# Performance work log

Hardware: AMD Instinct MI355X
Metric: run time of the kernel (lower is better)

The kernel has to match this reference:

```python
import jax, jax.numpy as jnp
import numpy as np

NUM_HEADS = 8
FREQ_RATIO = 0.5


def _resize_bilinear(img, out_h, out_w):
    """Bilinear resize of last two dims, matching torch interpolate align_corners=False."""
    in_h, in_w = img.shape[-2], img.shape[-1]

    def idx(in_size, out_size):
        src = jnp.maximum((jnp.arange(out_size, dtype=jnp.float32) + 0.5) * (in_size / out_size) - 0.5, 0.0)
        i0 = jnp.floor(src).astype(jnp.int32)
        i1 = jnp.minimum(i0 + 1, in_size - 1)
        w = src - i0.astype(jnp.float32)
        return i0, i1, w

    r0, r1, wr = idx(in_h, out_h)
    img = img[..., r0, :] * (1.0 - wr)[:, None] + img[..., r1, :] * wr[:, None]
    c0, c1, wc = idx(in_w, out_w)
    img = img[..., c0] * (1.0 - wc) + img[..., c1] * wc
    return img


def setup_inputs() -> dict:
    key = jax.random.key(0)
    ks = jax.random.split(key, 6)
    B, T, J, C = 4, 256, 17, 512
    H = NUM_HEADS
    x = jax.random.normal(ks[0], (B, T, J, C), dtype=jnp.float32)
    att_map = jax.random.uniform(ks[1], (B, H, J, T, T), dtype=jnp.float32)
    weight = jax.random.uniform(ks[2], (1,), dtype=jnp.float32)
    w_qkv = jax.random.normal(ks[3], (C, 3 * C), dtype=jnp.float32) * 0.02
    w_proj = jax.random.normal(ks[4], (C, C), dtype=jnp.float32) * 0.02
    b_proj = jnp.zeros((C,), dtype=jnp.float32)
    freq_gate = jnp.ones((1,), dtype=jnp.float32)
    return {"x": x, "att_map": att_map, "weight": weight, "w_qkv": w_qkv,
            "w_proj": w_proj, "b_proj": b_proj, "freq_gate": freq_gate}


def reference(x, att_map, weight, w_qkv, w_proj, b_proj, freq_gate):
    B, T, J, C = x.shape
    H = NUM_HEADS
    d = C // H
    scale = d ** (-0.5)

    qkv = (x @ w_qkv).reshape(B, T, J, 3, H, d)
    qkv = jnp.transpose(qkv, (3, 0, 4, 2, 1, 5))  # [3,B,H,J,T,d]
    q, k, v = qkv[0], qkv[1], qkv[2]

    # time-domain attention over T, per (B,H,J)
    attn_time = jax.nn.softmax(jnp.einsum('bhjtd,bhjsd->bhjts', q, k) * scale, axis=-1)

    # frequency-domain attention
    qf = jnp.fft.rfft(q, axis=3)
    kf = jnp.fft.rfft(k, axis=3)
    F = qf.shape[3]                      # T//2 + 1
    keep = max(1, int(F * FREQ_RATIO))
    qf = qf[:, :, :, :keep]
    kf = kf[:, :, :, :keep]
    af = jnp.einsum('bhjfd,bhjgd->bhjfg', qf, jnp.conj(kf)) * scale  # complex [B,H,J,keep,keep]
    # torch combines softmax(real) + 1j*softmax(imag); only the real part survives
    af_real = jax.nn.softmax(af.real, axis=-1)
    af_real = jnp.pad(af_real, ((0, 0), (0, 0), (0, 0), (0, F - keep), (0, 0)))  # zero-pad rows to F
    attn_freq = _resize_bilinear(af_real, T, T)  # [B,H,J,T,T]

    gate = jax.nn.sigmoid(freq_gate)  # broadcastable scalar
    attn_self = gate * attn_freq + (1.0 - gate) * attn_time
    attn = weight * attn_self + (1.0 - weight) * att_map

    out = jnp.einsum('bhjts,bhjsd->bhjtd', attn, v)        # [B,H,J,T,d]
    out = jnp.transpose(out, (0, 3, 2, 1, 4)).reshape(B, T, J, C)
    return out @ w_proj + b_proj
```

## Files before the change

kernel.cpp:

```cpp
#include <hip/hip_runtime.h>
#include <hip/hip_bf16.h>


#define SCALE 0.125f
#define LSTR 72

typedef __attribute__((ext_vector_type(4))) float f32x4;
typedef __attribute__((ext_vector_type(8))) short bf16x8;
typedef __attribute__((ext_vector_type(8))) unsigned short u16x8;

__device__ __forceinline__ float bf2f(unsigned short u) {
  return __uint_as_float(((unsigned int)u) << 16);
}
__device__ __forceinline__ unsigned short f2bf(float f) {
  unsigned int u = __float_as_uint(f);
  u += 0x7FFFu + ((u >> 16) & 1u);
  return (unsigned short)(u >> 16);
}

__global__ __launch_bounds__(256) void conv_x(
    const float* __restrict__ x, unsigned short* __restrict__ xh,
    unsigned short* __restrict__ xl) {
  const size_t i = ((size_t)blockIdx.x * 256 + threadIdx.x) * 8;
  float4 a = *(const float4*)(x + i);
  float4 b = *(const float4*)(x + i + 4);
  float vv[8] = {a.x, a.y, a.z, a.w, b.x, b.y, b.z, b.w};
  u16x8 hi, lo;
#pragma unroll
  for (int e = 0; e < 8; ++e) {
    unsigned short h = f2bf(vv[e]);
    hi[e] = h;
    lo[e] = f2bf(vv[e] - bf2f(h));
  }
  *(u16x8*)&xh[i] = hi;
  *(u16x8*)&xl[i] = lo;
}

__global__ __launch_bounds__(256) void conv_wT(
    const float* __restrict__ w, unsigned short* __restrict__ th,
    unsigned short* __restrict__ tl, int N) {
  __shared__ float T[64][65];
  const int tid = threadIdx.x;
  const int nt = blockIdx.x * 64, kt = blockIdx.y * 64;
  for (int i = tid; i < 4096; i += 256) {
    const int r = i >> 6, c = i & 63;
    T[r][c] = w[(size_t)(kt + r) * N + nt + c];
  }
  __syncthreads();
  for (int i = tid; i < 4096; i += 256) {
    const int rn = i >> 6, ck = i & 63;
    const float v = T[ck][rn];
    const unsigned short h = f2bf(v);
    const size_t o = (size_t)(nt + rn) * 512 + kt + ck;
    th[o] = h;
    tl[o] = f2bf(v - bf2f(h));
  }
}

__global__ __launch_bounds__(256, 2) void qkv_gemm(
    const unsigned short* __restrict__ xh, const unsigned short* __restrict__ xl,
    const unsigned short* __restrict__ wh, const unsigned short* __restrict__ wl,
    unsigned short* __restrict__ qh, unsigned short* __restrict__ ql,
    unsigned short* __restrict__ kh, unsigned short* __restrict__ kl,
    unsigned short* __restrict__ vt) {
  __shared__ __attribute__((aligned(16))) unsigned short Wt[2][128 * LSTR];
  __shared__ __attribute__((aligned(16))) unsigned short Xt[2][128 * LSTR];

  const int tid = threadIdx.x;
  const int bx = blockIdx.x, by = blockIdx.y;
  const int wid = tid >> 6, lane = tid & 63;
  const int lr = lane & 15, lg = lane >> 4;
  const int wr = wid >> 1, wc = wid & 1;
  const int srow = tid >> 3, skg = tid & 7;

  const unsigned short* xhp = xh + (size_t)(by * 128 + srow) * 512 + skg * 8;
  const unsigned short* xlp = xl + (size_t)(by * 128 + srow) * 512 + skg * 8;
  const unsigned short* whp = wh + (size_t)(bx * 128 + srow) * 512 + skg * 8;
  const unsigned short* wlp = wl + (size_t)(bx * 128 + srow) * 512 + skg * 8;

  u16x8 rxh[4], rxl[4], rwh[4], rwl[4];
  auto loadk = [&](int k0) {
#pragma unroll
    for (int it = 0; it < 4; ++it) {
      const size_t o = (size_t)(32 * it) * 512 + k0;
      rxh[it] = *(const u16x8*)(xhp + o);
      rxl[it] = *(const u16x8*)(xlp + o);
      rwh[it] = *(const u16x8*)(whp + o);
      rwl[it] = *(const u16x8*)(wlp + o);
    }
  };

  f32x4 acc[4][4];
#pragma unroll
  for (int nt = 0; nt < 4; ++nt)
#pragma unroll
    for (int mt = 0; mt < 4; ++mt) acc[nt][mt] = (f32x4){0.f, 0.f, 0.f, 0.f};

  loadk(0);
  for (int s = 0; s < 8; ++s) {
    if (s) __syncthreads();
#pragma unroll
    for (int it = 0; it < 4; ++it) {
      const int base = (srow + 32 * it) * LSTR + skg * 8;
      *(u16x8*)&Xt[0][base] = rxh[it];
      *(u16x8*)&Xt[1][base] = rxl[it];
      *(u16x8*)&Wt[0][base] = rwh[it];
      *(u16x8*)&Wt[1][base] = rwl[it];
    }
    __syncthreads();
    if (s < 7) loadk((s + 1) * 64);
#pragma unroll
    for (int kh2 = 0; kh2 < 2; ++kh2) {
      const int kbase = kh2 * 32 + lg * 8;
      bf16x8 Ah[4], Al[4], Bh[4], Bl[4];
#pragma unroll
      for (int nt = 0; nt < 4; ++nt) {
        const int n = wr * 64 + nt * 16 + lr;
        Ah[nt] = *(bf16x8*)&Wt[0][n * LSTR + kbase];
        Al[nt] = *(bf16x8*)&Wt[1][n * LSTR + kbase];
      }
#pragma unroll
      for (int mt = 0; mt < 4; ++mt) {
        const int m = wc * 64 + mt * 16 + lr;
        Bh[mt] = *(bf16x8*)&Xt[0][m * LSTR + kbase];
        Bl[mt] = *(bf16x8*)&Xt[1][m * LSTR + kbase];
      }
#pragma unroll
      for (int nt = 0; nt < 4; ++nt)
#pragma unroll
        for (int mt = 0; mt < 4; ++mt) {
          acc[nt][mt] = __builtin_amdgcn_mfma_f32_16x16x32_bf16(Ah[nt], Bh[mt], acc[nt][mt], 0, 0, 0);
          acc[nt][mt] = __builtin_amdgcn_mfma_f32_16x16x32_bf16(Ah[nt], Bl[mt], acc[nt][mt], 0, 0, 0);
          acc[nt][mt] = __builtin_amdgcn_mfma_f32_16x16x32_bf16(Al[nt], Bh[mt], acc[nt][mt], 0, 0, 0);
        }
    }
  }

#pragma unroll
  for (int mt = 0; mt < 4; ++mt) {
    const int m = by * 128 + wc * 64 + mt * 16 + lr;
    const int jj = m % 17;
    const int bt = m / 17;
    const int t = bt & 255;
    const int b = bt >> 8;
#pragma unroll
    for (int nt = 0; nt < 4; ++nt) {
      const int c = bx * 128 + wr * 64 + nt * 16 + lg * 4;
      const int qi = c >> 9;
      const int h = (c >> 6) & 7;
      const int dd = c & 63;
      const size_t hdbase = ((size_t)((b * 8 + h) * 17 + jj)) * 16384;
      float a0 = acc[nt][mt][0], a1 = acc[nt][mt][1], a2 = acc[nt][mt][2],
            a3 = acc[nt][mt][3];
      ushort4 hi4 = make_ushort4(f2bf(a0), f2bf(a1), f2bf(a2), f2bf(a3));
      if (qi == 2) {
        vt[hdbase + (size_t)(dd + 0) * 256 + t] = hi4.x;
        vt[hdbase + (size_t)(dd + 1) * 256 + t] = hi4.y;
        vt[hdbase + (size_t)(dd + 2) * 256 + t] = hi4.z;
        vt[hdbase + (size_t)(dd + 3) * 256 + t] = hi4.w;
      } else {
        ushort4 lo4 = make_ushort4(f2bf(a0 - bf2f(hi4.x)), f2bf(a1 - bf2f(hi4.y)),
                                   f2bf(a2 - bf2f(hi4.z)), f2bf(a3 - bf2f(hi4.w)));
        unsigned short* dh = qi ? kh : qh;
        unsigned short* dl = qi ? kl : ql;
        *(ushort4*)&dh[hdbase + t * 64 + dd] = hi4;
        *(ushort4*)&dl[hdbase + t * 64 + dd] = lo4;
      }
    }
  }
}

__global__ __launch_bounds__(256) void freq_kernel(
    const unsigned short* __restrict__ qhp, const unsigned short* __restrict__ qlp,
    const unsigned short* __restrict__ khp, const unsigned short* __restrict__ klp,
    unsigned short* __restrict__ af_out) {
  __shared__ __attribute__((aligned(16))) unsigned short qT[2][64 * 256];
  __shared__ __attribute__((aligned(16))) unsigned short QF[4][64 * 64];
  __shared__ __attribute__((aligned(16))) unsigned short KF[4][64 * 64];

  const int tid = threadIdx.x;
  const int head = blockIdx.x;
  const int w = tid >> 6, lane = tid & 63;
  const int lr = lane & 15, lg = lane >> 4;
  const int f0 = w << 4;

  bf16x8 Ech[8], Ecl[8], Esh[8], Esl[8];
  {
    const int f = f0 + lr;
#pragma unroll
    for (int kb = 0; kb < 8; ++kb) {
      bf16x8 ch, cl, sh, sl;
#pragma unroll
      for (int i = 0; i < 8; ++i) {
        int t = kb * 32 + lg * 8 + i;
        int idx = (f * t) & 255;
        float s, c;
        __sincosf((float)idx * 0.02454369260617026f, &s, &c);
        unsigned short chh = f2bf(c);
        unsigned short shh = f2bf(s);
        ch[i] = (short)chh;
        cl[i] = (short)f2bf(c - bf2f(chh));
        sh[i] = (short)shh;
        sl[i] = (short)f2bf(s - bf2f(shh));
      }
      Ech[kb] = ch; Ecl[kb] = cl; Esh[kb] = sh; Esl[kb] = sl;
    }
  }

  for (int pass = 0; pass < 2; ++pass) {
    const unsigned short* sh_ = (pass ? khp : qhp) + head * 16384;
    const unsigned short* sl_ = (pass ? klp : qlp) + head * 16384;
    __syncthreads();
    for (int i = tid; i < 4096; i += 256) {
      int t = i >> 4, dq = i & 15;
      ushort4 hv = *(const ushort4*)&sh_[t * 64 + dq * 4];
      ushort4 lv = *(const ushort4*)&sl_[t * 64 + dq * 4];
      unsigned short hvv[4] = {hv.x, hv.y, hv.z, hv.w};
      unsigned short lvv[4] = {lv.x, lv.y, lv.z, lv.w};
#pragma unroll
      for (int c = 0; c < 4; ++c) {
        int d = dq * 4 + c;
        int byo = d * 512 + ((t * 2) ^ ((d & 31) << 4));
        *(unsigned short*)((char*)qT[0] + byo) = hvv[c];
        *(unsigned short*)((char*)qT[1] + byo) = lvv[c];
      }
    }
    __syncthreads();

    f32x4 ar[4], ai[4];
#pragma unroll
    for (int nt = 0; nt < 4; ++nt) {
      ar[nt] = (f32x4){0.f, 0.f, 0.f, 0.f};
      ai[nt] = (f32x4){0.f, 0.f, 0.f, 0.f};
    }
#pragma unroll
    for (int kb = 0; kb < 8; ++kb) {
#pragma unroll
      for (int nt = 0; nt < 4; ++nt) {
        const int d = nt * 16 + lr;
        const int byo = d * 512 + ((kb * 64 + lg * 16) ^ ((d & 31) << 4));
        bf16x8 bh = *(bf16x8*)((char*)qT[0] + byo);
        bf16x8 bl = *(bf16x8*)((char*)qT[1] + byo);
        ar[nt] = __builtin_amdgcn_mfma_f32_16x16x32_bf16(Ech[kb], bh, ar[nt], 0, 0, 0);
        ar[nt] = __builtin_amdgcn_mfma_f32_16x16x32_bf16(Ech[kb], bl, ar[nt], 0, 0, 0);
        ar[nt] = __builtin_amdgcn_mfma_f32_16x16x32_bf16(Ecl[kb], bh, ar[nt], 0, 0, 0);
        ai[nt] = __builtin_amdgcn_mfma_f32_16x16x32_bf16(Esh[kb], bh, ai[nt], 0, 0, 0);
        ai[nt] = __builtin_amdgcn_mfma_f32_16x16x32_bf16(Esh[kb], bl, ai[nt], 0, 0, 0);
        ai[nt] = __builtin_amdgcn_mfma_f32_16x16x32_bf16(Esl[kb], bh, ai[nt], 0, 0, 0);
      }
    }
    unsigned short(*DST)[64 * 64] = pass ? KF : QF;
#pragma unroll
    for (int nt = 0; nt < 4; ++nt) {
#pragma unroll
      for (int j = 0; j < 4; ++j) {
        const int f = f0 + lg * 4 + j;
        const int d = nt * 16 + lr;
        const int byo = f * 128 + ((d * 2) ^ ((f & 7) << 4));
        float vr = ar[nt][j], vi = ai[nt][j];
        unsigned short rh = f2bf(vr);
        unsigned short ih = f2bf(vi);
        *(unsigned short*)((char*)DST[0] + byo) = rh;
        *(unsigned short*)((char*)DST[1] + byo) = f2bf(vr - bf2f(rh));
        *(unsigned short*)((char*)DST[2] + byo) = ih;
        *(unsigned short*)((char*)DST[3] + byo) = f2bf(vi - bf2f(ih));
      }
    }
  }
  __syncthreads();

  f32x4 acc[4];
#pragma unroll
  for (int nt = 0; nt < 4; ++nt) acc[nt] = (f32x4){0.f, 0.f, 0.f, 0.f};
#pragma unroll
  for (int kb = 0; kb < 2; ++kb) {
    const int fA = f0 + lr;
    const int abyo = fA * 128 + ((kb * 64 + lg * 16) ^ ((fA & 7) << 4));
    bf16x8 arh = *(bf16x8*)((char*)QF[0] + abyo);
    bf16x8 arl = *(bf16x8*)((char*)QF[1] + abyo);
    bf16x8 aih = *(bf16x8*)((char*)QF[2] + abyo);
    bf16x8 ail = *(bf16x8*)((char*)QF[3] + abyo);
#pragma unroll
    for (int nt = 0; nt < 4; ++nt) {
      const int g = nt * 16 + lr;
      const int bbyo = g * 128 + ((kb * 64 + lg * 16) ^ ((g & 7) << 4));
      bf16x8 brh = *(bf16x8*)((char*)KF[0] + bbyo);
      bf16x8 brl = *(bf16x8*)((char*)KF[1] + bbyo);
      bf16x8 bih = *(bf16x8*)((char*)KF[2] + bbyo);
      bf16x8 bil = *(bf16x8*)((char*)KF[3] + bbyo);
      acc[nt] = __builtin_amdgcn_mfma_f32_16x16x32_bf16(arh, brh, acc[nt], 0, 0, 0);
      acc[nt] = __builtin_amdgcn_mfma_f32_16x16x32_bf16(arh, brl, acc[nt], 0, 0, 0);
      acc[nt] = __builtin_amdgcn_mfma_f32_16x16x32_bf16(arl, brh, acc[nt], 0, 0, 0);
      acc[nt] = __builtin_amdgcn_mfma_f32_16x16x32_bf16(aih, bih, acc[nt], 0, 0, 0);
      acc[nt] = __builtin_amdgcn_mfma_f32_16x16x32_bf16(aih, bil, acc[nt], 0, 0, 0);
      acc[nt] = __builtin_amdgcn_mfma_f32_16x16x32_bf16(ail, bih, acc[nt], 0, 0, 0);
    }
  }

  unsigned short* outh = af_out + head * 4096;
#pragma unroll
  for (int j = 0; j < 4; ++j) {
    float m = fmaxf(fmaxf(acc[0][j], acc[1][j]), fmaxf(acc[2][j], acc[3][j]));
#pragma unroll
    for (int mask = 1; mask < 16; mask <<= 1) m = fmaxf(m, __shfl_xor(m, mask));
    float e[4];
    float rs = 0.f;
#pragma unroll
    for (int nt = 0; nt < 4; ++nt) {
      e[nt] = __expf((acc[nt][j] - m) * SCALE);
      rs += e[nt];
    }
#pragma unroll
    for (int mask = 1; mask < 16; mask <<= 1) rs += __shfl_xor(rs, mask);
    const float inv = 1.0f / rs;
    const int f = f0 + lg * 4 + j;
#pragma unroll
    for (int nt = 0; nt < 4; ++nt) outh[f * 64 + nt * 16 + lr] = f2bf(e[nt] * inv);
  }
}

__global__ __launch_bounds__(256) void attn_kernel(
    const unsigned short* __restrict__ qhp, const unsigned short* __restrict__ khp,
    const unsigned short* __restrict__ vtp, const unsigned short* __restrict__ af,
    const float* __restrict__ att_map, const float* __restrict__ weight,
    const float* __restrict__ fgate, float* __restrict__ out_perm) {
  __shared__ unsigned short Ks[256 * 64];
  __shared__ unsigned short Vt[64 * 256];
  __shared__ unsigned short afl[64 * 66];
  __shared__ unsigned short Psc[4][16 * 40];

  const int tid = threadIdx.x;
  const int head = blockIdx.x;
  const int jj = head % 17;
  const int hb = head / 17;
  const int h = hb & 7;
  const int b = hb >> 3;
  const int w = tid >> 6, lane = tid & 63;
  const int lr = lane & 15, lg = lane >> 4;

  const float* amh = att_map + (size_t)head * 65536;
  const unsigned short* qbase = qhp + head * 16384;

  bf16x8 rq[2];
  {
    const unsigned short* qrow = qbase + (w * 64 + lr) * 64 + lg * 8;
    rq[0] = *(const bf16x8*)(qrow);
    rq[1] = *(const bf16x8*)(qrow + 32);
  }

  const unsigned short* ksrc = khp + head * 16384;
  const unsigned short* vsrc = vtp + head * 16384;
  for (int i = tid; i < 2048; i += 256) {
    int s = i >> 3, dq8 = i & 7;
    u16x8 kv = *(const u16x8*)&ksrc[s * 64 + dq8 * 8];
    int koff = s * 128 + ((dq8 * 16) ^ ((s & 7) << 4));
    *(u16x8*)((char*)Ks + koff) = kv;
    int d = i >> 5, t8 = i & 31;
    u16x8 vv = *(const u16x8*)&vsrc[d * 256 + t8 * 8];
    int voff = d * 512 + ((t8 * 16) ^ ((d & 7) << 4));
    *(u16x8*)((char*)Vt + voff) = vv;
  }
  const unsigned short* asrc = af + head * 4096;
  for (int i = tid; i < 1024; i += 256) {
    int f = i >> 4, gq = (i & 15) << 2;
    *(ushort4*)&afl[f * 66 + gq] = *(const ushort4*)&asrc[f * 64 + gq];
  }
  __syncthreads();

  const float wv = weight[0];
  const float gate = 1.0f / (1.0f + __expf(-fgate[0]));
  unsigned short* psc = Psc[w];

  for (int tt = 0; tt < 4; ++tt) {
    const int tw = w * 64 + tt * 16;

    bf16x8 aq[2] = {rq[0], rq[1]};

    f32x4 S[16];
#pragma unroll
    for (int nt = 0; nt < 16; ++nt) {
      f32x4 accv = {0.f, 0.f, 0.f, 0.f};
#pragma unroll
      for (int kc = 0; kc < 2; ++kc) {
        int srow = nt * 16 + lr;
        int d0 = kc * 32 + lg * 8;
        int off = srow * 128 + ((d0 * 2) ^ ((srow & 7) << 4));
        bf16x8 bk = *(bf16x8*)((char*)Ks + off);
        accv = __builtin_amdgcn_mfma_f32_16x16x32_bf16(aq[kc], bk, accv, 0, 0, 0);
      }
      S[nt] = accv;
    }

    if (tt < 3) {
      const unsigned short* qrow = qbase + (tw + 16 + lr) * 64 + lg * 8;
      rq[0] = *(const bf16x8*)(qrow);
      rq[1] = *(const bf16x8*)(qrow + 32);
    }

    float inv[4], mrow[4];
#pragma unroll
    for (int j = 0; j < 4; ++j) {
      float m = -1e30f;
#pragma unroll
      for (int nt = 0; nt < 16; ++nt) m = fmaxf(m, S[nt][j]);
#pragma unroll
      for (int mask = 1; mask < 16; mask <<= 1) m = fmaxf(m, __shfl_xor(m, mask));
      mrow[j] = m;
    }
#pragma unroll
    for (int j = 0; j < 4; ++j) {
      float rs = 0.f;
#pragma unroll
      for (int nt = 0; nt < 16; ++nt) {
        float e = __expf((S[nt][j] - mrow[j]) * SCALE);
        S[nt][j] = e;
        rs += e;
      }
#pragma unroll
      for (int mask = 1; mask < 16; mask <<= 1) rs += __shfl_xor(rs, mask);
      inv[j] = 1.0f / rs;
    }

#pragma unroll
    for (int j = 0; j < 4; ++j) {
      const int t = tw + lg * 4 + j;
      float srcf = fmaxf((t + 0.5f) * (129.0f / 256.0f) - 0.5f, 0.0f);
      int f0r = (int)srcf;
      float wf = srcf - (float)f0r;
      int f1r = f0r + 1;
      if (f1r > 128) f1r = 128;
      const bool v0 = (f0r < 64), v1 = (f1r < 64);
#pragma unroll
      for (int nt = 0; nt < 16; ++nt) {
        const int s = nt * 16 + lr;
        float am = amh[t * 256 + s];
        float srcg = fmaxf((s + 0.5f) * 0.25f - 0.5f, 0.0f);
        int g0 = (int)srcg;
        float wc = srcg - (float)g0;
        int g1 = g0 + 1;
        if (g1 > 63) g1 = 63;
        float fr = 0.f;
        if (v0)
          fr += (1.0f - wf) *
                (bf2f(afl[f0r * 66 + g0]) * (1.0f - wc) + bf2f(afl[f0r * 66 + g1]) * wc);
        if (v1)
          fr += wf *
                (bf2f(afl[f1r * 66 + g0]) * (1.0f - wc) + bf2f(afl[f1r * 66 + g1]) * wc);
        float pt = S[nt][j] * inv[j];
        S[nt][j] = wv * (gate * fr + (1.0f - gate) * pt) + (1.0f - wv) * am;
      }
    }

    f32x4 O[4];
#pragma unroll
    for (int dt = 0; dt < 4; ++dt) O[dt] = (f32x4){0.f, 0.f, 0.f, 0.f};
#pragma unroll
    for (int sb = 0; sb < 8; ++sb) {
#pragma unroll
      for (int half = 0; half < 2; ++half) {
        const int nt = sb * 2 + half;
#pragma unroll
        for (int j = 0; j < 4; ++j) {
          psc[(lg * 4 + j) * 40 + half * 16 + lr] = f2bf(S[nt][j]);
        }
      }
      bf16x8 pa = *(bf16x8*)&psc[lr * 40 + lg * 8];
      const int s0 = sb * 32 + lg * 8;
#pragma unroll
      for (int dt = 0; dt < 4; ++dt) {
        const int d = dt * 16 + lr;
        int off = d * 512 + ((s0 * 2) ^ ((d & 7) << 4));
        bf16x8 bv = *(bf16x8*)((char*)Vt + off);
        O[dt] = __builtin_amdgcn_mfma_f32_16x16x32_bf16(pa, bv, O[dt], 0, 0, 0);
      }
    }

#pragma unroll
    for (int j = 0; j < 4; ++j) {
      const int t = tw + lg * 4 + j;
      float* orow = out_perm + ((size_t)((b * 256 + t) * 17 + jj)) * 512 + h * 64;
#pragma unroll
      for (int dt = 0; dt < 4; ++dt) {
        orow[dt * 16 + lr] = O[dt][j];
      }
    }
  }
}

__global__ __launch_bounds__(256, 2) void proj_gemm(
    const float* __restrict__ A,
    const unsigned short* __restrict__ wh, const unsigned short* __restrict__ wl,
    const float* __restrict__ bias, float* __restrict__ out) {
  __shared__ __attribute__((aligned(16))) unsigned short Wt[2][128 * LSTR];
  __shared__ __attribute__((aligned(16))) unsigned short Xt[2][128 * LSTR];

  const int tid = threadIdx.x;
  const int bx = blockIdx.x, by = blockIdx.y;
  const int wid = tid >> 6, lane = tid & 63;
  const int lr = lane & 15, lg = lane >> 4;
  const int wr = wid >> 1, wc = wid & 1;
  const int srow = tid >> 3, skg = tid & 7;

  const float* ap = A + (size_t)(by * 128 + srow) * 512 + skg * 8;
  const unsigned short* whp = wh + (size_t)(bx * 128 + srow) * 512 + skg * 8;
  const unsigned short* wlp = wl + (size_t)(bx * 128 + srow) * 512 + skg * 8;

  float4 rA[4][2];
  u16x8 rwh[4], rwl[4];
  auto loadk = [&](int k0) {
#pragma unroll
    for (int it = 0; it < 4; ++it) {
      const size_t o = (size_t)(32 * it) * 512 + k0;
      rA[it][0] = *(const float4*)(ap + o);
      rA[it][1] = *(const float4*)(ap + o + 4);
      rwh[it] = *(const u16x8*)(whp + o);
      rwl[it] = *(const u16x8*)(wlp + o);
    }
  };

  f32x4 acc[4][4];
#pragma unroll
  for (int nt = 0; nt < 4; ++nt)
#pragma unroll
    for (int mt = 0; mt < 4; ++mt) acc[nt][mt] = (f32x4){0.f, 0.f, 0.f, 0.f};

  loadk(0);
  for (int s = 0; s < 8; ++s) {
    if (s) __syncthreads();
#pragma unroll
    for (int it = 0; it < 4; ++it) {
      const int base = (srow + 32 * it) * LSTR + skg * 8;
      float vv[8] = {rA[it][0].x, rA[it][0].y, rA[it][0].z, rA[it][0].w,
                     rA[it][1].x, rA[it][1].y, rA[it][1].z, rA[it][1].w};
      u16x8 hi, lo;
#pragma unroll
      for (int e = 0; e < 8; ++e) {
        unsigned short h = f2bf(vv[e]);
        hi[e] = h;
        lo[e] = f2bf(vv[e] - bf2f(h));
      }
      *(u16x8*)&Xt[0][base] = hi;
      *(u16x8*)&Xt[1][base] = lo;
      *(u16x8*)&Wt[0][base] = rwh[it];
      *(u16x8*)&Wt[1][base] = rwl[it];
    }
    __syncthreads();
    if (s < 7) loadk((s + 1) * 64);
#pragma unroll
    for (int kh2 = 0; kh2 < 2; ++kh2) {
      const int kbase = kh2 * 32 + lg * 8;
      bf16x8 Ah[4], Al[4], Bh[4], Bl[4];
#pragma unroll
      for (int nt = 0; nt < 4; ++nt) {
        const int n = wr * 64 + nt * 16 + lr;
        Ah[nt] = *(bf16x8*)&Wt[0][n * LSTR + kbase];
        Al[nt] = *(bf16x8*)&Wt[1][n * LSTR + kbase];
      }
#pragma unroll
      for (int mt = 0; mt < 4; ++mt) {
        const int m = wc * 64 + mt * 16 + lr;
        Bh[mt] = *(bf16x8*)&Xt[0][m * LSTR + kbase];
        Bl[mt] = *(bf16x8*)&Xt[1][m * LSTR + kbase];
      }
#pragma unroll
      for (int nt = 0; nt < 4; ++nt)
#pragma unroll
        for (int mt = 0; mt < 4; ++mt) {
          acc[nt][mt] = __builtin_amdgcn_mfma_f32_16x16x32_bf16(Ah[nt], Bh[mt], acc[nt][mt], 0, 0, 0);
          acc[nt][mt] = __builtin_amdgcn_mfma_f32_16x16x32_bf16(Ah[nt], Bl[mt], acc[nt][mt], 0, 0, 0);
          acc[nt][mt] = __builtin_amdgcn_mfma_f32_16x16x32_bf16(Al[nt], Bh[mt], acc[nt][mt], 0, 0, 0);
        }
    }
  }

#pragma unroll
  for (int mt = 0; mt < 4; ++mt) {
    const int m = by * 128 + wc * 64 + mt * 16 + lr;
#pragma unroll
    for (int nt = 0; nt < 4; ++nt) {
      const int n = bx * 128 + wr * 64 + nt * 16 + lg * 4;
      float4 bi = *(const float4*)&bias[n];
      *(float4*)&out[(size_t)m * 512 + n] =
          make_float4(acc[nt][mt][0] + bi.x, acc[nt][mt][1] + bi.y,
                      acc[nt][mt][2] + bi.z, acc[nt][mt][3] + bi.w);
    }
  }
}

extern "C" void kernel_launch(void* const* d_in, const int* in_sizes, int n_in,
                              void* d_out, int out_size, void* d_ws, size_t ws_size,
                              hipStream_t stream) {
  (void)in_sizes; (void)n_in; (void)out_size; (void)ws_size;
  const float* x = (const float*)d_in[0];
  const float* att_map = (const float*)d_in[1];
  const float* weight = (const float*)d_in[2];
  const float* w_qkv = (const float*)d_in[3];
  const float* w_proj = (const float*)d_in[4];
  const float* b_proj = (const float*)d_in[5];
  const float* fgate = (const float*)d_in[6];
  float* out = (float*)d_out;

  char* ws = (char*)d_ws;
  const size_t PB = 17825792;
  unsigned short* qh = (unsigned short*)(ws);
  unsigned short* ql = (unsigned short*)(ws + PB);
  unsigned short* kh = (unsigned short*)(ws + 2 * PB);
  unsigned short* kl = (unsigned short*)(ws + 3 * PB);
  unsigned short* vt = (unsigned short*)(ws + 4 * PB);
  unsigned short* af = (unsigned short*)(ws + 5 * PB);
  char* base = ws + 5 * PB + 4456448;
  unsigned short* xh = (unsigned short*)(base);
  unsigned short* xl = (unsigned short*)(base + PB);
  float* out_perm = (float*)(base);
  unsigned short* wqh = (unsigned short*)(base + 35651584);
  unsigned short* wql = (unsigned short*)(base + 35651584 + 1572864);
  unsigned short* wph = (unsigned short*)(base + 35651584 + 2 * 1572864);
  unsigned short* wpl = (unsigned short*)(base + 35651584 + 2 * 1572864 + 524288);

  conv_x<<<4352, 256, 0, stream>>>(x, xh, xl);
  conv_wT<<<dim3(24, 8), 256, 0, stream>>>(w_qkv, wqh, wql, 1536);
  conv_wT<<<dim3(8, 8), 256, 0, stream>>>(w_proj, wph, wpl, 512);
  qkv_gemm<<<dim3(12, 136), 256, 0, stream>>>(xh, xl, wqh, wql, qh, ql, kh, kl, vt);
  freq_kernel<<<544, 256, 0, stream>>>(qh, ql, kh, kl, af);
  attn_kernel<<<544, 256, 0, stream>>>(qh, kh, vt, af, att_map, weight, fgate,
                                       out_perm);
  proj_gemm<<<dim3(4, 136), 256, 0, stream>>>(out_perm, wph, wpl, b_proj, out);
}
```

Baseline: 409.3 us.

## Precompute column-resized freq attention times V, apply row interpolation after PV

The frequency-attention term is rewritten using linearity. Each of the 64 kept frequency rows is column-interpolated once and multiplied by V with MFMA, giving a 64x64 matrix stored in shared memory. The per-row interpolation is then applied to the output rows, so the 256x256 bilinear expansion per head is no longer built inside the softmax loop. The att_map reads are changed to vectorized float4 loads, prefetched one step ahead and blended into the P operand. Precision shifts slightly because the af@V product is rounded to bf16, and an extra precompute phase with two block barriers is added.

```diff
diff --git a/kernel.cpp b/kernel.cpp
--- a/kernel.cpp
+++ b/kernel.cpp
@@ -326,7 +326,7 @@
     const float* __restrict__ fgate, float* __restrict__ out_perm) {
   __shared__ unsigned short Ks[256 * 64];
   __shared__ unsigned short Vt[64 * 256];
-  __shared__ unsigned short afl[64 * 66];
+  __shared__ unsigned short AFW[64 * 66];
   __shared__ unsigned short Psc[4][16 * 40];
 
   const int tid = threadIdx.x;
@@ -340,13 +340,6 @@
 
   const float* amh = att_map + (size_t)head * 65536;
   const unsigned short* qbase = qhp + head * 16384;
-
-  bf16x8 rq[2];
-  {
-    const unsigned short* qrow = qbase + (w * 64 + lr) * 64 + lg * 8;
-    rq[0] = *(const bf16x8*)(qrow);
-    rq[1] = *(const bf16x8*)(qrow + 32);
-  }
 
   const unsigned short* ksrc = khp + head * 16384;
   const unsigned short* vsrc = vtp + head * 16384;
@@ -363,16 +356,66 @@
   const unsigned short* asrc = af + head * 4096;
   for (int i = tid; i < 1024; i += 256) {
     int f = i >> 4, gq = (i & 15) << 2;
-    *(ushort4*)&afl[f * 66 + gq] = *(const ushort4*)&asrc[f * 64 + gq];
+    *(ushort4*)&AFW[f * 66 + gq] = *(const ushort4*)&asrc[f * 64 + gq];
   }
   __syncthreads();
 
   const float wv = weight[0];
   const float gate = 1.0f / (1.0f + __expf(-fgate[0]));
+  const float cg = wv * gate;
+  const float cp = wv * (1.0f - gate);
+  const float c2 = 1.0f - wv;
   unsigned short* psc = Psc[w];
+
+  {
+    const int fA = w * 16 + lr;
+    f32x4 wacc[4];
+#pragma unroll
+    for (int nt = 0; nt < 4; ++nt) wacc[nt] = (f32x4){0.f, 0.f, 0.f, 0.f};
+#pragma unroll
+    for (int kc = 0; kc < 8; ++kc) {
+      bf16x8 afr;
+#pragma unroll
+      for (int i = 0; i < 8; ++i) {
+        const int s = kc * 32 + lg * 8 + i;
+        float srcg = fmaxf((s + 0.5f) * 0.25f - 0.5f, 0.0f);
+        int g0 = (int)srcg;
+        float wc = srcg - (float)g0;
+        int g1 = g0 + 1;
+        if (g1 > 63) g1 = 63;
+        float v = bf2f(AFW[fA * 66 + g0]) * (1.0f - wc) + bf2f(AFW[fA * 66 + g1]) * wc;
+        afr[i] = (short)f2bf(v);
+      }
+      const int s0 = kc * 32 + lg * 8;
+#pragma unroll
+      for (int nt = 0; nt < 4; ++nt) {
+        const int d = nt * 16 + lr;
+        const int off = d * 512 + ((s0 * 2) ^ ((d & 7) << 4));
+        bf16x8 bv = *(bf16x8*)((char*)Vt + off);
+        wacc[nt] = __builtin_amdgcn_mfma_f32_16x16x32_bf16(afr, bv, wacc[nt], 0, 0, 0);
+      }
+    }
+    __syncthreads();
+#pragma unroll
+    for (int nt = 0; nt < 4; ++nt) {
+#pragma unroll
+      for (int j = 0; j < 4; ++j) {
+        AFW[(w * 16 + lg * 4 + j) * 66 + nt * 16 + lr] = f2bf(wacc[nt][j]);
+      }
+    }
+    __syncthreads();
+  }
+
+  bf16x8 rq[2];
+  {
+    const unsigned short* qrow = qbase + (w * 64 + lr) * 64 + lg * 8;
+    rq[0] = *(const bf16x8*)(qrow);
+    rq[1] = *(const bf16x8*)(qrow + 32);
+  }
 
   for (int tt = 0; tt < 4; ++tt) {
     const int tw = w * 64 + tt * 16;
+    const float* amrow = amh + (size_t)(tw + lr) * 256 + lg * 8;
 
     bf16x8 aq[2] = {rq[0], rq[1]};
 
@@ -397,7 +440,7 @@
       rq[1] = *(const bf16x8*)(qrow + 32);
     }
 
-    float inv[4], mrow[4];
+    float c1j[4];
 #pragma unroll
     for (int j = 0; j < 4; ++j) {
       float m = -1e30f;
@@ -405,20 +448,57 @@
       for (int nt = 0; nt < 16; ++nt) m = fmaxf(m, S[nt][j]);
 #pragma unroll
       for (int mask = 1; mask < 16; mask <<= 1) m = fmaxf(m, __shfl_xor(m, mask));
-      mrow[j] = m;
-    }
-#pragma unroll
-    for (int j = 0; j < 4; ++j) {
       float rs = 0.f;
 #pragma unroll
       for (int nt = 0; nt < 16; ++nt) {
-        float e = __expf((S[nt][j] - mrow[j]) * SCALE);
+        float e = __expf((S[nt][j] - m) * SCALE);
         S[nt][j] = e;
         rs += e;
       }
 #pragma unroll
       for (int mask = 1; mask < 16; mask <<= 1) rs += __shfl_xor(rs, mask);
-      inv[j] = 1.0f / rs;
+      c1j[j] = cp / rs;
+    }
+
+    f32x4 O[4];
+#pragma unroll
+    for (int dt = 0; dt < 4; ++dt) O[dt] = (f32x4){0.f, 0.f, 0.f, 0.f};
+    float4 am0 = *(const float4*)(amrow);
+    float4 am1 = *(const float4*)(amrow + 4);
+#pragma unroll
+    for (int sb = 0; sb < 8; ++sb) {
+      float4 nx0, nx1;
+      if (sb < 7) {
+        nx0 = *(const float4*)(amrow + (sb + 1) * 32);
+        nx1 = *(const float4*)(amrow + (sb + 1) * 32 + 4);
+      }
+#pragma unroll
+      for (int half = 0; half < 2; ++half) {
+        const int nt = sb * 2 + half;
+#pragma unroll
+        for (int j = 0; j < 4; ++j) {
+          psc[(lg * 4 + j) * 40 + half * 16 + lr] = f2bf(c1j[j] * S[nt][j]);
+        }
+      }
+      bf16x8 praw = *(bf16x8*)&psc[lr * 40 + lg * 8];
+      bf16x8 pa;
+      {
+        float av[8] = {am0.x, am0.y, am0.z, am0.w, am1.x, am1.y, am1.z, am1.w};
+#pragma unroll
+        for (int i = 0; i < 8; ++i) {
+          pa[i] = (short)f2bf(bf2f((unsigned short)praw[i]) + c2 * av[i]);
+        }
+      }
+      const int s0 = sb * 32 + lg * 8;
+#pragma unroll
+      for (int dt = 0; dt < 4; ++dt) {
+        const int d = dt * 16 + lr;
+        int off = d * 512 + ((s0 * 2) ^ ((d & 7) << 4));
+        bf16x8 bv = *(bf16x8*)((char*)Vt + off);
+        O[dt] = __builtin_amdgcn_mfma_f32_16x16x32_bf16(pa, bv, O[dt], 0, 0, 0);
+      }
+      am0 = nx0;
+      am1 = nx1;
     }
 
 #pragma unroll
@@ -428,60 +508,15 @@
       int f0r = (int)srcf;
       float wf = srcf - (float)f0r;
       int f1r = f0r + 1;
-      if (f1r > 128) f1r = 128;
       const bool v0 = (f0r < 64), v1 = (f1r < 64);
-#pragma unroll
-      for (int nt = 0; nt < 16; ++nt) {
-        const int s = nt * 16 + lr;
-        float am = amh[t * 256 + s];
-        float srcg = fmaxf((s + 0.5f) * 0.25f - 0.5f, 0.0f);
-        int g0 = (int)srcg;
-        float wc = srcg - (float)g0;
-        int g1 = g0 + 1;
-        if (g1 > 63) g1 = 63;
-        float fr = 0.f;
-        if (v0)
-          fr += (1.0f - wf) *
-                (bf2f(afl[f0r * 66 + g0]) * (1.0f - wc) + bf2f(afl[f0r * 66 + g1]) * wc);
-        if (v1)
-          fr += wf *
-                (bf2f(afl[f1r * 66 + g0]) * (1.0f - wc) + bf2f(afl[f1r * 66 + g1]) * wc);
-        float pt = S[nt][j] * inv[j];
-        S[nt][j] = wv * (gate * fr + (1.0f - gate) * pt) + (1.0f - wv) * am;
-      }
-    }
-
-    f32x4 O[4];
-#pragma unroll
-    for (int dt = 0; dt < 4; ++dt) O[dt] = (f32x4){0.f, 0.f, 0.f, 0.f};
-#pragma unroll
-    for (int sb = 0; sb < 8; ++sb) {
-#pragma unroll
-      for (int half = 0; half < 2; ++half) {
-        const int nt = sb * 2 + half;
-#pragma unroll
-        for (int j = 0; j < 4; ++j) {
-          psc[(lg * 4 + j) * 40 + half * 16 + lr] = f2bf(S[nt][j]);
-        }
-      }
-      bf16x8 pa = *(bf16x8*)&psc[lr * 40 + lg * 8];
-      const int s0 = sb * 32 + lg * 8;
+      float* orow = out_perm + ((size_t)((b * 256 + t) * 17 + jj)) * 512 + h * 64;
 #pragma unroll
       for (int dt = 0; dt < 4; ++dt) {
         const int d = dt * 16 + lr;
-        int off = d * 512 + ((s0 * 2) ^ ((d & 7) << 4));
-        bf16x8 bv = *(bf16x8*)((char*)Vt + off);
-        O[dt] = __builtin_amdgcn_mfma_f32_16x16x32_bf16(pa, bv, O[dt], 0, 0, 0);
-      }
-    }
-
-#pragma unroll
-    for (int j = 0; j < 4; ++j) {
-      const int t = tw + lg * 4 + j;
-      float* orow = out_perm + ((size_t)((b * 256 + t) * 17 + jj)) * 512 + h * 64;
-#pragma unroll
-      for (int dt = 0; dt < 4; ++dt) {
-        orow[dt * 16 + lr] = O[dt][j];
+        float fv = 0.f;
+        if (v0) fv += (1.0f - wf) * bf2f(AFW[f0r * 66 + d]);
+        if (v1) fv += wf * bf2f(AFW[f1r * 66 + d]);
+        orow[d] = O[dt][j] + cg * fv;
       }
     }
   }
```

After: 379.1 us. -7.4%, faster.
